# Kernel tuning notes

Hardware: AMD Instinct MI355X
Metric: run time of the kernel (lower is better)

The kernel has to match this reference:

```python
import jax, jax.numpy as jnp
import numpy as np

N_ATOMS = 8_000_000
N_REC = 2_000_000
N_POC = 500_000
N_CHAINS = 4


def setup_inputs() -> dict:
    key = jax.random.key(0)
    k1, k2, k3, k4 = jax.random.split(key, 4)
    # coordinates in nm, inside a ~5 nm box
    positions = jax.random.uniform(k1, (N_ATOMS, 3), dtype=jnp.float32) * 5.0
    box_vectors = jnp.diag(jnp.array([5.0, 5.0, 5.0], dtype=jnp.float32))
    # unique receptor atom indices into positions
    rec_indices = jax.random.permutation(k2, N_ATOMS)[:N_REC].astype(jnp.int32)
    # unique pocket indices INTO THE REC ARRAY (poc_pos = rec_pos[poc_indices])
    poc_indices = jax.random.permutation(k3, N_REC)[:N_POC].astype(jnp.int32)
    # contiguous chain assignment over rec atoms, all chains present in pocket
    chain_ids = ((jnp.arange(N_REC, dtype=jnp.int32) * N_CHAINS) // N_REC).astype(jnp.int32)
    poc_chain_ids = chain_ids[poc_indices]
    ref_poc = jax.random.uniform(k4, (N_POC, 3), dtype=jnp.float32) * 5.0
    k = jnp.float32(100.0)  # kJ/mol/nm^2
    return {
        "positions": positions, "box_vectors": box_vectors, "ref_poc": ref_poc,
        "k": k, "rec_indices": rec_indices, "poc_indices": poc_indices,
        "chain_ids": chain_ids, "poc_chain_ids": poc_chain_ids, "n_chains": N_CHAINS,
    }


def best_periodic_translation(pos1, pos2, box_vectors):
    # pos1, pos2: [C,3]; box_vectors: [3,3] (rows are lattice vectors)
    delta = pos2 - pos1
    inv = 1.0 / jnp.diag(box_vectors)
    s3 = jnp.round(delta[:, 2] * inv[2])
    delta = delta - s3[:, None] * box_vectors[2]
    s2 = jnp.round(delta[:, 1] * inv[1])
    delta = delta - s2[:, None] * box_vectors[1]
    s1 = jnp.round(delta[:, 0] * inv[0])
    return s1[:, None] * box_vectors[0] + s2[:, None] * box_vectors[1] + s3[:, None] * box_vectors[2]


def reference(positions, box_vectors, ref_poc, k, rec_indices, poc_indices, chain_ids, poc_chain_ids, n_chains):
    rec_pos = positions[rec_indices]  # [R,3]
    # Per-chain pocket COM. NOTE: original indexes global positions here
    # (positions[poc_chain_indices]), NOT rec_pos -- reproduced faithfully.
    poc_glob = positions[poc_indices]  # [P,3]
    counts = jax.ops.segment_sum(jnp.ones((poc_glob.shape[0],), poc_glob.dtype), poc_chain_ids, num_segments=n_chains)  # [C]
    poc_com = jax.ops.segment_sum(poc_glob, poc_chain_ids, num_segments=n_chains) / counts[:, None]  # [C,3]
    ref_com = jax.ops.segment_sum(ref_poc, poc_chain_ids, num_segments=n_chains) / counts[:, None]  # [C,3]
    best_t = best_periodic_translation(poc_com, ref_com, box_vectors)  # [C,3]
    rec_pos = rec_pos + best_t[chain_ids]  # translate each chain into the reference image

    poc_pos = rec_pos[poc_indices]  # [P,3]
    rec_origin = jnp.mean(rec_pos, axis=0)
    rec_centered = rec_pos - rec_origin
    r_sq = jnp.sum(rec_centered ** 2, axis=1)  # [R]
    F = jnp.zeros_like(rec_pos).at[poc_indices].set(-2.0 * k * (poc_pos - ref_poc))
    F_mean = jnp.mean(F, axis=0)
    torque = jnp.cross(rec_centered, F)
    torque_mean = jnp.mean(torque, axis=0)
    F_rot = jnp.cross(torque_mean[None], rec_centered) / r_sq[:, None]
    F_final = jnp.zeros_like(positions).at[rec_indices].set(F_mean + F_rot)
    return (jnp.float32(0.0), F_final)
```

## Files before the change

### kernel.cpp

```cpp
#include <hip/hip_runtime.h>


typedef unsigned int uint32;
typedef unsigned char uchar;

#define MAXC 16
#define W_BT 0
#define W_O 48
#define W_FM 52
#define W_TM 56
#define W_ACC 64

#define GCOUNT_OFF 4096
#define REC_OFF 8192
#define NB 512
#define BSH 14
#define BUCKET_ATOMS (1 << BSH)
#define CAP 5120
#define INV8_OFF (REC_OFF + NB * CAP * 4)

#define PB 512
#define K1_KPT 16
#define K1_CHUNK (256 * K1_KPT)

struct PocSh  { float accL[3 + MAXC * 10]; };
struct MapSh  { uchar map_[BUCKET_ATOMS]; };
union ShU { PocSh poc; MapSh map; };

__device__ inline float waveSum(float v) {
#pragma unroll
  for (int off = 32; off > 0; off >>= 1) v += __shfl_down(v, off, 64);
  return v;
}

__global__ __launch_bounds__(256) void k_partition(
    const int* __restrict__ rec_idx, const int* __restrict__ cid,
    int R, uint32* __restrict__ gcount, uint32* __restrict__ grecords) {
  __shared__ uint32 hist[NB];
  __shared__ uint32 curs[NB];
  __shared__ uint32 base[NB];
  const int tid = threadIdx.x;
  const int r0 = blockIdx.x * K1_CHUNK;
  int cnt = R - r0; if (cnt > K1_CHUNK) cnt = K1_CHUNK;
  for (int t = tid; t < NB; t += 256) { hist[t] = 0u; curs[t] = 0u; }
  __syncthreads();
  uint32 enc[K1_KPT];
#pragma unroll
  for (int j = 0; j < K1_KPT; ++j) {
    int t = tid + j * 256;
    uint32 e = 0xFFFFFFFFu;
    if (t < cnt) {
      uint32 idx = (uint32)rec_idx[r0 + t];
      uint32 c = (uint32)cid[r0 + t] & 255u;
      e = (idx << 8) | c;
      atomicAdd(&hist[idx >> BSH], 1u);
    }
    enc[j] = e;
  }
  __syncthreads();
  for (int t = tid; t < NB; t += 256) {
    uint32 h = hist[t];
    base[t] = h ? atomicAdd(&gcount[t], h) : 0u;
  }
  __syncthreads();
#pragma unroll
  for (int j = 0; j < K1_KPT; ++j) {
    uint32 e = enc[j];
    if (e != 0xFFFFFFFFu) {
      uint32 b = e >> (8 + BSH);
      uint32 slot = base[b] + atomicAdd(&curs[b], 1u);
      if (slot < CAP) grecords[b * CAP + slot] = e;
    }
  }
}

__global__ __launch_bounds__(256) void k_gather(
    const float* __restrict__ pos, const float* __restrict__ ref_poc,
    const int* __restrict__ rec_idx,
    const int* __restrict__ poc_idx, const int* __restrict__ poc_cid,
    const int* __restrict__ ncp, int P, int N,
    const uint32* __restrict__ gcount, const uint32* __restrict__ grecords,
    uchar* __restrict__ inv8, float* __restrict__ ws) {
  const int tid = threadIdx.x;
  const int bid = blockIdx.x;
  const int C = ncp[0];
  __shared__ ShU sh;
  __shared__ float red[4][43];
  __shared__ float cnt16[MAXC];

  if ((bid & 1) == 0) {
    const int pt = bid >> 1;
    const int gsz = PB * 256;
    if (C <= 4) {
      float vals[43];
#pragma unroll
      for (int v = 0; v < 43; ++v) vals[v] = 0.f;
      for (int rb = pt * 256 + tid; rb < P; rb += 4 * gsz) {
        int rr[4], i2[4], c2[4], ri[4];
        float g[4][3], p[4][3], rf[4][3];
#pragma unroll
        for (int q = 0; q < 4; ++q) {
          int r = rb + q * gsz;
          rr[q] = (r < P) ? r : -1;
        }
#pragma unroll
        for (int q = 0; q < 4; ++q) {
          int r = (rr[q] < 0) ? 0 : rr[q];
          i2[q] = poc_idx[r];
          c2[q] = poc_cid[r];
        }
#pragma unroll
        for (int q = 0; q < 4; ++q) {
          ri[q] = rec_idx[i2[q]];
          g[q][0] = pos[3 * i2[q] + 0];
          g[q][1] = pos[3 * i2[q] + 1];
          g[q][2] = pos[3 * i2[q] + 2];
        }
#pragma unroll
        for (int q = 0; q < 4; ++q) {
          int r = (rr[q] < 0) ? 0 : rr[q];
          p[q][0] = pos[3 * ri[q] + 0];
          p[q][1] = pos[3 * ri[q] + 1];
          p[q][2] = pos[3 * ri[q] + 2];
          rf[q][0] = ref_poc[3 * r + 0];
          rf[q][1] = ref_poc[3 * r + 1];
          rf[q][2] = ref_poc[3 * r + 2];
        }
#pragma unroll
        for (int q = 0; q < 4; ++q) {
          if (rr[q] >= 0) {
            vals[0] += p[q][1] * rf[q][2] - p[q][2] * rf[q][1];
            vals[1] += p[q][2] * rf[q][0] - p[q][0] * rf[q][2];
            vals[2] += p[q][0] * rf[q][1] - p[q][1] * rf[q][0];
#pragma unroll
            for (int cc = 0; cc < 4; ++cc) {
              bool m = (c2[q] == cc);
              float* a = &vals[3 + cc * 10];
              a[0] += m ? g[q][0] : 0.f; a[1] += m ? g[q][1] : 0.f;
              a[2] += m ? g[q][2] : 0.f;
              a[3] += m ? rf[q][0] : 0.f; a[4] += m ? rf[q][1] : 0.f;
              a[5] += m ? rf[q][2] : 0.f;
              a[6] += m ? p[q][0] : 0.f; a[7] += m ? p[q][1] : 0.f;
              a[8] += m ? p[q][2] : 0.f;
              a[9] += m ? 1.f : 0.f;
            }
          }
        }
      }
      const int wid = tid >> 6;
#pragma unroll
      for (int v = 0; v < 43; ++v) {
        float s = waveSum(vals[v]);
        if ((tid & 63) == 0) red[wid][v] = s;
      }
      __syncthreads();
      for (int t = tid; t < 43; t += 256)
        atomicAdd(&ws[W_ACC + 19 + t],
                  red[0][t] + red[1][t] + red[2][t] + red[3][t]);
    } else {
      float* accL = sh.poc.accL;
      for (int t = tid; t < 3 + MAXC * 10; t += 256) accL[t] = 0.f;
      __syncthreads();
      for (int r = pt * 256 + tid; r < P; r += PB * 256) {
        int i2 = poc_idx[r];
        int c2 = poc_cid[r];
        int ri = rec_idx[i2];
        float gx = pos[3 * i2 + 0], gy = pos[3 * i2 + 1], gz = pos[3 * i2 + 2];
        float px = pos[3 * ri + 0], py = pos[3 * ri + 1], pz = pos[3 * ri + 2];
        float rx = ref_poc[3 * r + 0], ry = ref_poc[3 * r + 1], rz = ref_poc[3 * r + 2];
        atomicAdd(&accL[0], py * rz - pz * ry);
        atomicAdd(&accL[1], pz * rx - px * rz);
        atomicAdd(&accL[2], px * ry - py * rx);
        float* a = &accL[3 + c2 * 10];
        atomicAdd(&a[0], gx); atomicAdd(&a[1], gy); atomicAdd(&a[2], gz);
        atomicAdd(&a[3], rx); atomicAdd(&a[4], ry); atomicAdd(&a[5], rz);
        atomicAdd(&a[6], px); atomicAdd(&a[7], py); atomicAdd(&a[8], pz);
        atomicAdd(&a[9], 1.f);
      }
      __syncthreads();
      for (int t = tid; t < 3 + MAXC * 10; t += 256)
        if (accL[t] != 0.f) atomicAdd(&ws[W_ACC + 19 + t], accL[t]);
    }
  } else {
    const int b = bid >> 1;
    const int a0 = b << BSH;
    if (a0 >= N) return;
    int natoms = N - a0; if (natoms > BUCKET_ATOMS) natoms = BUCKET_ATOMS;
    uchar* map_ = sh.map.map_;
    uint4* m16 = (uint4*)map_;
    uint4 ff; ff.x = ff.y = ff.z = ff.w = 0xFFFFFFFFu;
    for (int t = tid; t < BUCKET_ATOMS / 16; t += 256) m16[t] = ff;
    if (C > 4) for (int t = tid; t < MAXC; t += 256) cnt16[t] = 0.f;
    __syncthreads();
    int n = (int)gcount[b]; if (n > CAP) n = CAP;
    float c0 = 0.f, c1 = 0.f, c2 = 0.f, c3 = 0.f;
    for (int t = tid; t < n; t += 256) {
      uint32 e = grecords[b * CAP + t];
      uint32 ia = (e >> 8) & (BUCKET_ATOMS - 1);
      uint32 c = e & 255u;
      map_[ia] = (uchar)c;
      if (C <= 4) {
        c0 += (c == 0u) ? 1.f : 0.f;
        c1 += (c == 1u) ? 1.f : 0.f;
        c2 += (c == 2u) ? 1.f : 0.f;
        c3 += (c == 3u) ? 1.f : 0.f;
      } else {
        atomicAdd(&cnt16[c], 1.f);
      }
    }
    __syncthreads();
    uchar* dst = inv8 + a0;
    if (natoms == BUCKET_ATOMS) {
      uint4* d16 = (uint4*)dst;
      for (int t = tid; t < BUCKET_ATOMS / 16; t += 256) d16[t] = m16[t];
    } else {
      for (int t = tid; t < natoms; t += 256) dst[t] = map_[t];
    }
    float sx = 0.f, sy = 0.f, sz = 0.f;
    int ngf = natoms >> 2;
    const uchar4* m4 = (const uchar4*)map_;
    const float4* pos4 = (const float4*)pos;
    int g0 = a0 >> 2;
    for (int g = tid; g < ngf; g += 256) {
      float4 p0 = pos4[3 * (g0 + g) + 0];
      float4 p1 = pos4[3 * (g0 + g) + 1];
      float4 p2 = pos4[3 * (g0 + g) + 2];
      uchar4 m = m4[g];
      if (m.x != 255) { sx += p0.x; sy += p0.y; sz += p0.z; }
      if (m.y != 255) { sx += p0.w; sy += p1.x; sz += p1.y; }
      if (m.z != 255) { sx += p1.z; sy += p1.w; sz += p2.x; }
      if (m.w != 255) { sx += p2.y; sy += p2.z; sz += p2.w; }
    }
    int tb = natoms & 3;
    if (tid < tb) {
      int a = a0 + (ngf << 2) + tid;
      if (map_[(ngf << 2) + tid] != 255) {
        sx += pos[3 * a]; sy += pos[3 * a + 1]; sz += pos[3 * a + 2];
      }
    }
    float vv[7] = {sx, sy, sz, c0, c1, c2, c3};
    const int wid = tid >> 6;
#pragma unroll
    for (int v = 0; v < 7; ++v) {
      float s = waveSum(vv[v]);
      if ((tid & 63) == 0) red[wid][v] = s;
    }
    __syncthreads();
    if (tid < 7) {
      float s = red[0][tid] + red[1][tid] + red[2][tid] + red[3][tid];
      atomicAdd(&ws[W_ACC + tid], s);
    }
    if (C > 4 && tid < C) atomicAdd(&ws[W_ACC + 3 + tid], cnt16[tid]);
  }
}

__global__ __launch_bounds__(256) void k_finout(
    const float* __restrict__ pos, const uchar* __restrict__ inv8,
    const float* __restrict__ box, const float* __restrict__ kp,
    const int* __restrict__ ncp, int R, int N,
    const float* __restrict__ ws, float* __restrict__ out) {
  __shared__ float stage[3328];
  __shared__ float tot[192];
  __shared__ float sc[64];
  const int tid = threadIdx.x;
  const int t0 = blockIdx.x * 1024;
  int nat = N - t0; if (nat > 1024) nat = 1024;
  const int nfl = nat * 3;

  for (int t = tid; t < 192; t += 256) tot[t] = ws[W_ACC + t];

  if (nat == 1024) {
    const float4* src4 = (const float4*)(pos + 3 * t0);
#pragma unroll
    for (int kk = 0; kk < 3; ++kk) {
      int v4 = tid + kk * 256;
      float4 p = src4[v4];
      int idx = 4 * v4 + v4 / 3;
      stage[idx + 0] = p.x; stage[idx + 1] = p.y;
      stage[idx + 2] = p.z; stage[idx + 3] = p.w;
    }
  } else {
    for (int k = tid; k < nfl; k += 256)
      stage[k + (int)((unsigned)k / 12u)] = pos[3 * t0 + k];
  }
  __syncthreads();

  if (tid == 0) {
    const int C = ncp[0];
    const float kk = kp[0];
    const float Rf = (float)R;
    const float* xp = &tot[19];
    float inv0 = 1.f / box[0], inv1 = 1.f / box[4], inv2 = 1.f / box[8];
    float ox = tot[0], oy = tot[1], oz = tot[2];
    float Fx = 0, Fy = 0, Fz = 0;
    float T1x = 0, T1y = 0, T1z = 0, T2x = 0, T2y = 0, T2z = 0;
    for (int c = 0; c < C; ++c) {
      float nrec = tot[3 + c];
      const float* a = &tot[22 + c * 10];
      float np = a[9];
      float invn = 1.f / np;
      float pcx = a[0] * invn, pcy = a[1] * invn, pcz = a[2] * invn;
      float rcx = a[3] * invn, rcy = a[4] * invn, rcz = a[5] * invn;
      float dx = rcx - pcx, dy = rcy - pcy, dz = rcz - pcz;
      float s3 = rintf(dz * inv2);
      dx -= s3 * box[6]; dy -= s3 * box[7]; dz -= s3 * box[8];
      float s2 = rintf(dy * inv1);
      dx -= s2 * box[3]; dy -= s2 * box[4]; dz -= s2 * box[5];
      float s1 = rintf(dx * inv0);
      float btx = s1 * box[0] + s2 * box[3] + s3 * box[6];
      float bty = s1 * box[1] + s2 * box[4] + s3 * box[7];
      float btz = s1 * box[2] + s2 * box[5] + s3 * box[8];
      sc[W_BT + c * 3 + 0] = btx;
      sc[W_BT + c * 3 + 1] = bty;
      sc[W_BT + c * 3 + 2] = btz;
      ox += nrec * btx; oy += nrec * bty; oz += nrec * btz;
      float SFx = -2.f * kk * (a[6] + np * btx - a[3]);
      float SFy = -2.f * kk * (a[7] + np * bty - a[4]);
      float SFz = -2.f * kk * (a[8] + np * btz - a[5]);
      Fx += SFx; Fy += SFy; Fz += SFz;
      T1x += a[7] * btz - a[8] * bty;
      T1y += a[8] * btx - a[6] * btz;
      T1z += a[6] * bty - a[7] * btx;
      T2x += bty * SFz - btz * SFy;
      T2y += btz * SFx - btx * SFz;
      T2z += btx * SFy - bty * SFx;
    }
    ox /= Rf; oy /= Rf; oz /= Rf;
    float Tx = 2.f * kk * xp[0] - 2.f * kk * T1x + T2x - (oy * Fz - oz * Fy);
    float Ty = 2.f * kk * xp[1] - 2.f * kk * T1y + T2y - (oz * Fx - ox * Fz);
    float Tz = 2.f * kk * xp[2] - 2.f * kk * T1z + T2z - (ox * Fy - oy * Fx);
    sc[W_O + 0] = ox; sc[W_O + 1] = oy; sc[W_O + 2] = oz;
    sc[W_FM + 0] = Fx / Rf; sc[W_FM + 1] = Fy / Rf; sc[W_FM + 2] = Fz / Rf;
    sc[W_TM + 0] = Tx / Rf; sc[W_TM + 1] = Ty / Rf; sc[W_TM + 2] = Tz / Rf;
  }
  __syncthreads();

  const float ox = sc[W_O + 0], oy = sc[W_O + 1], oz = sc[W_O + 2];
  const float fmx = sc[W_FM + 0], fmy = sc[W_FM + 1], fmz = sc[W_FM + 2];
  const float tmx = sc[W_TM + 0], tmy = sc[W_TM + 1], tmz = sc[W_TM + 2];

  uchar mc[4];
  if (nat == 1024) {
    uchar4 m = ((const uchar4*)(inv8 + t0))[tid];
    mc[0] = m.x; mc[1] = m.y; mc[2] = m.z; mc[3] = m.w;
  } else {
#pragma unroll
    for (int q = 0; q < 4; ++q) {
      int la = 4 * tid + q;
      mc[q] = (la < nat) ? inv8[t0 + la] : (uchar)255;
    }
  }
#pragma unroll
  for (int q = 0; q < 4; ++q) {
    int la = 4 * tid + q;
    if (la < nat) {
      float* s = &stage[13 * tid + 3 * q];
      float fx = 0.f, fy = 0.f, fz = 0.f;
      int c = mc[q];
      if (c != 255) {
        float cx = s[0] + sc[W_BT + 3 * c + 0] - ox;
        float cy = s[1] + sc[W_BT + 3 * c + 1] - oy;
        float cz = s[2] + sc[W_BT + 3 * c + 2] - oz;
        float inv = 1.f / (cx * cx + cy * cy + cz * cz);
        fx = fmx + (tmy * cz - tmz * cy) * inv;
        fy = fmy + (tmz * cx - tmx * cz) * inv;
        fz = fmz + (tmx * cy - tmy * cx) * inv;
      }
      s[0] = fx; s[1] = fy; s[2] = fz;
    }
  }
  __syncthreads();

  if (blockIdx.x == 0 && tid == 0) out[0] = 0.f;
  float* ob = out + 1 + 3 * t0;
  if (nat == 1024) {
#pragma unroll
    for (int kk = 0; kk < 3; ++kk) {
      int j = tid + kk * 256;
      if (j < 767) {
        int k = 3 + 4 * j;
        float4 v;
        v.x = stage[k + k / 12];
        v.y = stage[(k + 1) + (k + 1) / 12];
        v.z = stage[(k + 2) + (k + 2) / 12];
        v.w = stage[(k + 3) + (k + 3) / 12];
        *(float4*)(ob + k) = v;
      }
    }
    if (tid < 3) ob[tid] = stage[tid];
    if (tid == 3) ob[3071] = stage[3071 + 3071 / 12];
  } else {
    for (int k = tid; k < nfl; k += 256)
      ob[k] = stage[k + (int)((unsigned)k / 12u)];
  }
}

extern "C" void kernel_launch(void* const* d_in, const int* in_sizes, int n_in,
                              void* d_out, int out_size, void* d_ws, size_t ws_size,
                              hipStream_t stream) {
  const float* pos     = (const float*)d_in[0];
  const float* box     = (const float*)d_in[1];
  const float* ref_poc = (const float*)d_in[2];
  const float* kp      = (const float*)d_in[3];
  const int* rec_idx   = (const int*)d_in[4];
  const int* poc_idx   = (const int*)d_in[5];
  const int* cid       = (const int*)d_in[6];
  const int* poc_cid   = (const int*)d_in[7];
  const int* ncp       = (const int*)d_in[8];
  float* out = (float*)d_out;
  float* ws  = (float*)d_ws;
  uint32* gcount   = (uint32*)((char*)d_ws + GCOUNT_OFF);
  uint32* grecords = (uint32*)((char*)d_ws + REC_OFF);
  uchar*  inv8     = (uchar*)d_ws + INV8_OFF;

  const int N = in_sizes[0] / 3;
  const int R = in_sizes[4];
  const int P = in_sizes[5];

  hipMemsetAsync(d_ws, 0, 8192, stream);

  const int nchunk = (R + K1_CHUNK - 1) / K1_CHUNK;
  k_partition<<<nchunk, 256, 0, stream>>>(rec_idx, cid, R, gcount, grecords);
  k_gather<<<1024, 256, 0, stream>>>(pos, ref_poc, rec_idx, poc_idx, poc_cid,
                                     ncp, P, N, gcount, grecords, inv8, ws);
  int gF = (N + 1023) / 1024;
  k_finout<<<gF, 256, 0, stream>>>(pos, inv8, box, kp, ncp, R, N, ws, out);
}
```

Before: 270.2 us.

## Fuse three kernels into one persistent kernel with software grid barriers

```diff
diff --git a/kernel.cpp b/kernel.cpp
--- a/kernel.cpp
+++ b/kernel.cpp
@@ -11,6 +11,7 @@
 #define W_TM 56
 #define W_ACC 64
 
+#define BAR_OFF 4032
 #define GCOUNT_OFF 4096
 #define REC_OFF 8192
 #define NB 512
@@ -19,13 +20,18 @@
 #define CAP 5120
 #define INV8_OFF (REC_OFF + NB * CAP * 4)
 
-#define PB 512
+#define GRID 512
+#define PBK 256
 #define K1_KPT 16
 #define K1_CHUNK (256 * K1_KPT)
 
+#define SPIN_MAX (1 << 22)
+
+struct PartSh { uint32 hist[NB]; uint32 curs[NB]; uint32 base[NB]; };
 struct PocSh  { float accL[3 + MAXC * 10]; };
 struct MapSh  { uchar map_[BUCKET_ATOMS]; };
-union ShU { PocSh poc; MapSh map; };
+struct StageSh{ float stage[3328]; float tot[192]; };
+union ShU { PartSh part; PocSh poc; MapSh map; StageSh st; };
 
 __device__ inline float waveSum(float v) {
 #pragma unroll
@@ -33,64 +39,87 @@
   return v;
 }
 
-__global__ __launch_bounds__(256) void k_partition(
-    const int* __restrict__ rec_idx, const int* __restrict__ cid,
-    int R, uint32* __restrict__ gcount, uint32* __restrict__ grecords) {
-  __shared__ uint32 hist[NB];
-  __shared__ uint32 curs[NB];
-  __shared__ uint32 base[NB];
-  const int tid = threadIdx.x;
-  const int r0 = blockIdx.x * K1_CHUNK;
-  int cnt = R - r0; if (cnt > K1_CHUNK) cnt = K1_CHUNK;
-  for (int t = tid; t < NB; t += 256) { hist[t] = 0u; curs[t] = 0u; }
+__device__ inline void gridBar(uint32* bar, uint32 phase, int* shOk) {
+  __threadfence();
   __syncthreads();
-  uint32 enc[K1_KPT];
-#pragma unroll
-  for (int j = 0; j < K1_KPT; ++j) {
-    int t = tid + j * 256;
-    uint32 e = 0xFFFFFFFFu;
-    if (t < cnt) {
-      uint32 idx = (uint32)rec_idx[r0 + t];
-      uint32 c = (uint32)cid[r0 + t] & 255u;
-      e = (idx << 8) | c;
-      atomicAdd(&hist[idx >> BSH], 1u);
-    }
-    enc[j] = e;
+  if (threadIdx.x == 0) {
+    __hip_atomic_fetch_add(bar, 1u, __ATOMIC_ACQ_REL, __HIP_MEMORY_SCOPE_AGENT);
+    const uint32 tgt = (uint32)GRID * phase;
+    for (int it = 0; it < SPIN_MAX; ++it) {
+      if (__hip_atomic_load(bar, __ATOMIC_ACQUIRE, __HIP_MEMORY_SCOPE_AGENT) >= tgt)
+        break;
+      __builtin_amdgcn_s_sleep(2);
+    }
+    *shOk = 1;
   }
   __syncthreads();
-  for (int t = tid; t < NB; t += 256) {
-    uint32 h = hist[t];
-    base[t] = h ? atomicAdd(&gcount[t], h) : 0u;
-  }
-  __syncthreads();
-#pragma unroll
-  for (int j = 0; j < K1_KPT; ++j) {
-    uint32 e = enc[j];
-    if (e != 0xFFFFFFFFu) {
-      uint32 b = e >> (8 + BSH);
-      uint32 slot = base[b] + atomicAdd(&curs[b], 1u);
-      if (slot < CAP) grecords[b * CAP + slot] = e;
-    }
-  }
+  __threadfence();
 }
 
-__global__ __launch_bounds__(256) void k_gather(
+__global__ __launch_bounds__(256, 2) void k_all(
     const float* __restrict__ pos, const float* __restrict__ ref_poc,
-    const int* __restrict__ rec_idx,
+    const int* __restrict__ rec_idx, const int* __restrict__ cid,
     const int* __restrict__ poc_idx, const int* __restrict__ poc_cid,
-    const int* __restrict__ ncp, int P, int N,
-    const uint32* __restrict__ gcount, const uint32* __restrict__ grecords,
-    uchar* __restrict__ inv8, float* __restrict__ ws) {
+    const int* __restrict__ ncp, const float* __restrict__ box,
+    const float* __restrict__ kp, int R, int P, int N,
+    uint32* __restrict__ gcount, uint32* __restrict__ grecords,
+    uchar* __restrict__ inv8, float* __restrict__ ws,
+    float* __restrict__ out, uint32* __restrict__ bar) {
+  __shared__ ShU sh;
+  __shared__ float red[4][43];
+  __shared__ float cnt16[MAXC];
+  __shared__ float sc[64];
+  __shared__ int shOk;
   const int tid = threadIdx.x;
   const int bid = blockIdx.x;
   const int C = ncp[0];
-  __shared__ ShU sh;
-  __shared__ float red[4][43];
-  __shared__ float cnt16[MAXC];
+  const int NCHUNK = (R + K1_CHUNK - 1) / K1_CHUNK;
+
+  {
+    uint32* hist = sh.part.hist;
+    uint32* curs = sh.part.curs;
+    uint32* base = sh.part.base;
+    for (int ch = bid; ch < NCHUNK; ch += GRID) {
+      const int r0 = ch * K1_CHUNK;
+      int cnt = R - r0; if (cnt > K1_CHUNK) cnt = K1_CHUNK;
+      for (int t = tid; t < NB; t += 256) { hist[t] = 0u; curs[t] = 0u; }
+      __syncthreads();
+      uint32 enc[K1_KPT];
+#pragma unroll
+      for (int j = 0; j < K1_KPT; ++j) {
+        int t = tid + j * 256;
+        uint32 e = 0xFFFFFFFFu;
+        if (t < cnt) {
+          uint32 idx = (uint32)rec_idx[r0 + t];
+          uint32 c = (uint32)cid[r0 + t] & 255u;
+          e = (idx << 8) | c;
+          atomicAdd(&hist[idx >> BSH], 1u);
+        }
+        enc[j] = e;
+      }
+      __syncthreads();
+      for (int t = tid; t < NB; t += 256) {
+        uint32 h = hist[t];
+        base[t] = h ? atomicAdd(&gcount[t], h) : 0u;
+      }
+      __syncthreads();
+#pragma unroll
+      for (int j = 0; j < K1_KPT; ++j) {
+        uint32 e = enc[j];
+        if (e != 0xFFFFFFFFu) {
+          uint32 b = e >> (8 + BSH);
+          uint32 slot = base[b] + atomicAdd(&curs[b], 1u);
+          if (slot < CAP) grecords[b * CAP + slot] = e;
+        }
+      }
+      __syncthreads();
+    }
+  }
+  gridBar(bar, 1, &shOk);
 
   if ((bid & 1) == 0) {
     const int pt = bid >> 1;
-    const int gsz = PB * 256;
+    const int gsz = PBK * 256;
     if (C <= 4) {
       float vals[43];
 #pragma unroll
@@ -161,7 +190,7 @@
       float* accL = sh.poc.accL;
       for (int t = tid; t < 3 + MAXC * 10; t += 256) accL[t] = 0.f;
       __syncthreads();
-      for (int r = pt * 256 + tid; r < P; r += PB * 256) {
+      for (int r = pt * 256 + tid; r < P; r += PBK * 256) {
         int i2 = poc_idx[r];
         int c2 = poc_cid[r];
         int ri = rec_idx[i2];
@@ -182,216 +211,215 @@
         if (accL[t] != 0.f) atomicAdd(&ws[W_ACC + 19 + t], accL[t]);
     }
   } else {
-    const int b = bid >> 1;
-    const int a0 = b << BSH;
-    if (a0 >= N) return;
-    int natoms = N - a0; if (natoms > BUCKET_ATOMS) natoms = BUCKET_ATOMS;
-    uchar* map_ = sh.map.map_;
-    uint4* m16 = (uint4*)map_;
-    uint4 ff; ff.x = ff.y = ff.z = ff.w = 0xFFFFFFFFu;
-    for (int t = tid; t < BUCKET_ATOMS / 16; t += 256) m16[t] = ff;
-    if (C > 4) for (int t = tid; t < MAXC; t += 256) cnt16[t] = 0.f;
+    for (int b = (bid >> 1); b < NB; b += 256) {
+      const int a0 = b << BSH;
+      if (a0 >= N) break;
+      int natoms = N - a0; if (natoms > BUCKET_ATOMS) natoms = BUCKET_ATOMS;
+      uchar* map_ = sh.map.map_;
+      uint4* m16 = (uint4*)map_;
+      uint4 ff; ff.x = ff.y = ff.z = ff.w = 0xFFFFFFFFu;
+      for (int t = tid; t < BUCKET_ATOMS / 16; t += 256) m16[t] = ff;
+      if (C > 4) for (int t = tid; t < MAXC; t += 256) cnt16[t] = 0.f;
+      __syncthreads();
+      int n = (int)gcount[b]; if (n > CAP) n = CAP;
+      float c0 = 0.f, c1 = 0.f, c2 = 0.f, c3 = 0.f;
+      for (int t = tid; t < n; t += 256) {
+        uint32 e = grecords[b * CAP + t];
+        uint32 ia = (e >> 8) & (BUCKET_ATOMS - 1);
+        uint32 c = e & 255u;
+        map_[ia] = (uchar)c;
+        if (C <= 4) {
+          c0 += (c == 0u) ? 1.f : 0.f;
+          c1 += (c == 1u) ? 1.f : 0.f;
+          c2 += (c == 2u) ? 1.f : 0.f;
+          c3 += (c == 3u) ? 1.f : 0.f;
+        } else {
+          atomicAdd(&cnt16[c], 1.f);
+        }
+      }
+      __syncthreads();
+      uchar* dst = inv8 + a0;
+      if (natoms == BUCKET_ATOMS) {
+        uint4* d16 = (uint4*)dst;
+        for (int t = tid; t < BUCKET_ATOMS / 16; t += 256) d16[t] = m16[t];
+      } else {
+        for (int t = tid; t < natoms; t += 256) dst[t] = map_[t];
+      }
+      float sx = 0.f, sy = 0.f, sz = 0.f;
+      int ngf = natoms >> 2;
+      const uchar4* m4 = (const uchar4*)map_;
+      const float4* pos4 = (const float4*)pos;
+      int g0 = a0 >> 2;
+      for (int g = tid; g < ngf; g += 256) {
+        float4 p0 = pos4[3 * (g0 + g) + 0];
+        float4 p1 = pos4[3 * (g0 + g) + 1];
+        float4 p2 = pos4[3 * (g0 + g) + 2];
+        uchar4 m = m4[g];
+        if (m.x != 255) { sx += p0.x; sy += p0.y; sz += p0.z; }
+        if (m.y != 255) { sx += p0.w; sy += p1.x; sz += p1.y; }
+        if (m.z != 255) { sx += p1.z; sy += p1.w; sz += p2.x; }
+        if (m.w != 255) { sx += p2.y; sy += p2.z; sz += p2.w; }
+      }
+      int tb = natoms & 3;
+      if (tid < tb) {
+        int a = a0 + (ngf << 2) + tid;
+        if (map_[(ngf << 2) + tid] != 255) {
+          sx += pos[3 * a]; sy += pos[3 * a + 1]; sz += pos[3 * a + 2];
+        }
+      }
+      float vv[7] = {sx, sy, sz, c0, c1, c2, c3};
+      const int wid = tid >> 6;
+#pragma unroll
+      for (int v = 0; v < 7; ++v) {
+        float s = waveSum(vv[v]);
+        if ((tid & 63) == 0) red[wid][v] = s;
+      }
+      __syncthreads();
+      if (tid < 7) {
+        float s = red[0][tid] + red[1][tid] + red[2][tid] + red[3][tid];
+        atomicAdd(&ws[W_ACC + tid], s);
+      }
+      if (C > 4 && tid < C) atomicAdd(&ws[W_ACC + 3 + tid], cnt16[tid]);
+      __syncthreads();
+    }
+  }
+  gridBar(bar, 2, &shOk);
+
+  {
+    float* tot = sh.st.tot;
+    for (int t = tid; t < 192; t += 256) tot[t] = ws[W_ACC + t];
     __syncthreads();
-    int n = (int)gcount[b]; if (n > CAP) n = CAP;
-    float c0 = 0.f, c1 = 0.f, c2 = 0.f, c3 = 0.f;
-    for (int t = tid; t < n; t += 256) {
-      uint32 e = grecords[b * CAP + t];
-      uint32 ia = (e >> 8) & (BUCKET_ATOMS - 1);
-      uint32 c = e & 255u;
-      map_[ia] = (uchar)c;
-      if (C <= 4) {
-        c0 += (c == 0u) ? 1.f : 0.f;
-        c1 += (c == 1u) ? 1.f : 0.f;
-        c2 += (c == 2u) ? 1.f : 0.f;
-        c3 += (c == 3u) ? 1.f : 0.f;
+    if (tid == 0) {
+      const float kk = kp[0];
+      const float Rf = (float)R;
+      const float* xp = &tot[19];
+      float inv0 = 1.f / box[0], inv1 = 1.f / box[4], inv2 = 1.f / box[8];
+      float ox = tot[0], oy = tot[1], oz = tot[2];
+      float Fx = 0, Fy = 0, Fz = 0;
+      float T1x = 0, T1y = 0, T1z = 0, T2x = 0, T2y = 0, T2z = 0;
+      for (int c = 0; c < C; ++c) {
+        float nrec = tot[3 + c];
+        const float* a = &tot[22 + c * 10];
+        float np = a[9];
+        float invn = 1.f / np;
+        float pcx = a[0] * invn, pcy = a[1] * invn, pcz = a[2] * invn;
+        float rcx = a[3] * invn, rcy = a[4] * invn, rcz = a[5] * invn;
+        float dx = rcx - pcx, dy = rcy - pcy, dz = rcz - pcz;
+        float s3 = rintf(dz * inv2);
+        dx -= s3 * box[6]; dy -= s3 * box[7]; dz -= s3 * box[8];
+        float s2 = rintf(dy * inv1);
+        dx -= s2 * box[3]; dy -= s2 * box[4]; dz -= s2 * box[5];
+        float s1 = rintf(dx * inv0);
+        float btx = s1 * box[0] + s2 * box[3] + s3 * box[6];
+        float bty = s1 * box[1] + s2 * box[4] + s3 * box[7];
+        float btz = s1 * box[2] + s2 * box[5] + s3 * box[8];
+        sc[W_BT + c * 3 + 0] = btx;
+        sc[W_BT + c * 3 + 1] = bty;
+        sc[W_BT + c * 3 + 2] = btz;
+        ox += nrec * btx; oy += nrec * bty; oz += nrec * btz;
+        float SFx = -2.f * kk * (a[6] + np * btx - a[3]);
+        float SFy = -2.f * kk * (a[7] + np * bty - a[4]);
+        float SFz = -2.f * kk * (a[8] + np * btz - a[5]);
+        Fx += SFx; Fy += SFy; Fz += SFz;
+        T1x += a[7] * btz - a[8] * bty;
+        T1y += a[8] * btx - a[6] * btz;
+        T1z += a[6] * bty - a[7] * btx;
+        T2x += bty * SFz - btz * SFy;
+        T2y += btz * SFx - btx * SFz;
+        T2z += btx * SFy - bty * SFx;
+      }
+      ox /= Rf; oy /= Rf; oz /= Rf;
+      float Tx = 2.f * kk * xp[0] - 2.f * kk * T1x + T2x - (oy * Fz - oz * Fy);
+      float Ty = 2.f * kk * xp[1] - 2.f * kk * T1y + T2y - (oz * Fx - ox * Fz);
+      float Tz = 2.f * kk * xp[2] - 2.f * kk * T1z + T2z - (ox * Fy - oy * Fx);
+      sc[W_O + 0] = ox; sc[W_O + 1] = oy; sc[W_O + 2] = oz;
+      sc[W_FM + 0] = Fx / Rf; sc[W_FM + 1] = Fy / Rf; sc[W_FM + 2] = Fz / Rf;
+      sc[W_TM + 0] = Tx / Rf; sc[W_TM + 1] = Ty / Rf; sc[W_TM + 2] = Tz / Rf;
+    }
+    __syncthreads();
+    const float ox = sc[W_O + 0], oy = sc[W_O + 1], oz = sc[W_O + 2];
+    const float fmx = sc[W_FM + 0], fmy = sc[W_FM + 1], fmz = sc[W_FM + 2];
+    const float tmx = sc[W_TM + 0], tmy = sc[W_TM + 1], tmz = sc[W_TM + 2];
+
+    const int ntiles = (N + 1023) >> 10;
+    for (int tile = bid; tile < ntiles; tile += GRID) {
+      const int t0 = tile << 10;
+      int nat = N - t0; if (nat > 1024) nat = 1024;
+      const int nfl = nat * 3;
+      float* stage = sh.st.stage;
+
+      if (nat == 1024) {
+        const float4* src4 = (const float4*)(pos + 3 * t0);
+#pragma unroll
+        for (int kk = 0; kk < 3; ++kk) {
+          int v4 = tid + kk * 256;
+          float4 p = src4[v4];
+          int idx = 4 * v4 + v4 / 3;
+          stage[idx + 0] = p.x; stage[idx + 1] = p.y;
+          stage[idx + 2] = p.z; stage[idx + 3] = p.w;
+        }
       } else {
-        atomicAdd(&cnt16[c], 1.f);
-      }
-    }
-    __syncthreads();
-    uchar* dst = inv8 + a0;
-    if (natoms == BUCKET_ATOMS) {
-      uint4* d16 = (uint4*)dst;
-      for (int t = tid; t < BUCKET_ATOMS / 16; t += 256) d16[t] = m16[t];
-    } else {
-      for (int t = tid; t < natoms; t += 256) dst[t] = map_[t];
-    }
-    float sx = 0.f, sy = 0.f, sz = 0.f;
-    int ngf = natoms >> 2;
-    const uchar4* m4 = (const uchar4*)map_;
-    const float4* pos4 = (const float4*)pos;
-    int g0 = a0 >> 2;
-    for (int g = tid; g < ngf; g += 256) {
-      float4 p0 = pos4[3 * (g0 + g) + 0];
-      float4 p1 = pos4[3 * (g0 + g) + 1];
-      float4 p2 = pos4[3 * (g0 + g) + 2];
-      uchar4 m = m4[g];
-      if (m.x != 255) { sx += p0.x; sy += p0.y; sz += p0.z; }
-      if (m.y != 255) { sx += p0.w; sy += p1.x; sz += p1.y; }
-      if (m.z != 255) { sx += p1.z; sy += p1.w; sz += p2.x; }
-      if (m.w != 255) { sx += p2.y; sy += p2.z; sz += p2.w; }
-    }
-    int tb = natoms & 3;
-    if (tid < tb) {
-      int a = a0 + (ngf << 2) + tid;
-      if (map_[(ngf << 2) + tid] != 255) {
-        sx += pos[3 * a]; sy += pos[3 * a + 1]; sz += pos[3 * a + 2];
-      }
-    }
-    float vv[7] = {sx, sy, sz, c0, c1, c2, c3};
-    const int wid = tid >> 6;
-#pragma unroll
-    for (int v = 0; v < 7; ++v) {
-      float s = waveSum(vv[v]);
-      if ((tid & 63) == 0) red[wid][v] = s;
-    }
-    __syncthreads();
-    if (tid < 7) {
-      float s = red[0][tid] + red[1][tid] + red[2][tid] + red[3][tid];
-      atomicAdd(&ws[W_ACC + tid], s);
-    }
-    if (C > 4 && tid < C) atomicAdd(&ws[W_ACC + 3 + tid], cnt16[tid]);
-  }
-}
-
-__global__ __launch_bounds__(256) void k_finout(
-    const float* __restrict__ pos, const uchar* __restrict__ inv8,
-    const float* __restrict__ box, const float* __restrict__ kp,
-    const int* __restrict__ ncp, int R, int N,
-    const float* __restrict__ ws, float* __restrict__ out) {
-  __shared__ float stage[3328];
-  __shared__ float tot[192];
-  __shared__ float sc[64];
-  const int tid = threadIdx.x;
-  const int t0 = blockIdx.x * 1024;
-  int nat = N - t0; if (nat > 1024) nat = 1024;
-  const int nfl = nat * 3;
-
-  for (int t = tid; t < 192; t += 256) tot[t] = ws[W_ACC + t];
-
-  if (nat == 1024) {
-    const float4* src4 = (const float4*)(pos + 3 * t0);
-#pragma unroll
-    for (int kk = 0; kk < 3; ++kk) {
-      int v4 = tid + kk * 256;
-      float4 p = src4[v4];
-      int idx = 4 * v4 + v4 / 3;
-      stage[idx + 0] = p.x; stage[idx + 1] = p.y;
-      stage[idx + 2] = p.z; stage[idx + 3] = p.w;
-    }
-  } else {
-    for (int k = tid; k < nfl; k += 256)
-      stage[k + (int)((unsigned)k / 12u)] = pos[3 * t0 + k];
-  }
-  __syncthreads();
-
-  if (tid == 0) {
-    const int C = ncp[0];
-    const float kk = kp[0];
-    const float Rf = (float)R;
-    const float* xp = &tot[19];
-    float inv0 = 1.f / box[0], inv1 = 1.f / box[4], inv2 = 1.f / box[8];
-    float ox = tot[0], oy = tot[1], oz = tot[2];
-    float Fx = 0, Fy = 0, Fz = 0;
-    float T1x = 0, T1y = 0, T1z = 0, T2x = 0, T2y = 0, T2z = 0;
-    for (int c = 0; c < C; ++c) {
-      float nrec = tot[3 + c];
-      const float* a = &tot[22 + c * 10];
-      float np = a[9];
-      float invn = 1.f / np;
-      float pcx = a[0] * invn, pcy = a[1] * invn, pcz = a[2] * invn;
-      float rcx = a[3] * invn, rcy = a[4] * invn, rcz = a[5] * invn;
-      float dx = rcx - pcx, dy = rcy - pcy, dz = rcz - pcz;
-      float s3 = rintf(dz * inv2);
-      dx -= s3 * box[6]; dy -= s3 * box[7]; dz -= s3 * box[8];
-      float s2 = rintf(dy * inv1);
-      dx -= s2 * box[3]; dy -= s2 * box[4]; dz -= s2 * box[5];
-      float s1 = rintf(dx * inv0);
-      float btx = s1 * box[0] + s2 * box[3] + s3 * box[6];
-      float bty = s1 * box[1] + s2 * box[4] + s3 * box[7];
-      float btz = s1 * box[2] + s2 * box[5] + s3 * box[8];
-      sc[W_BT + c * 3 + 0] = btx;
-      sc[W_BT + c * 3 + 1] = bty;
-      sc[W_BT + c * 3 + 2] = btz;
-      ox += nrec * btx; oy += nrec * bty; oz += nrec * btz;
-      float SFx = -2.f * kk * (a[6] + np * btx - a[3]);
-      float SFy = -2.f * kk * (a[7] + np * bty - a[4]);
-      float SFz = -2.f * kk * (a[8] + np * btz - a[5]);
-      Fx += SFx; Fy += SFy; Fz += SFz;
-      T1x += a[7] * btz - a[8] * bty;
-      T1y += a[8] * btx - a[6] * btz;
-      T1z += a[6] * bty - a[7] * btx;
-      T2x += bty * SFz - btz * SFy;
-      T2y += btz * SFx - btx * SFz;
-      T2z += btx * SFy - bty * SFx;
-    }
-    ox /= Rf; oy /= Rf; oz /= Rf;
-    float Tx = 2.f * kk * xp[0] - 2.f * kk * T1x + T2x - (oy * Fz - oz * Fy);
-    float Ty = 2.f * kk * xp[1] - 2.f * kk * T1y + T2y - (oz * Fx - ox * Fz);
-    float Tz = 2.f * kk * xp[2] - 2.f * kk * T1z + T2z - (ox * Fy - oy * Fx);
-    sc[W_O + 0] = ox; sc[W_O + 1] = oy; sc[W_O + 2] = oz;
-    sc[W_FM + 0] = Fx / Rf; sc[W_FM + 1] = Fy / Rf; sc[W_FM + 2] = Fz / Rf;
-    sc[W_TM + 0] = Tx / Rf; sc[W_TM + 1] = Ty / Rf; sc[W_TM + 2] = Tz / Rf;
-  }
-  __syncthreads();
-
-  const float ox = sc[W_O + 0], oy = sc[W_O + 1], oz = sc[W_O + 2];
-  const float fmx = sc[W_FM + 0], fmy = sc[W_FM + 1], fmz = sc[W_FM + 2];
-  const float tmx = sc[W_TM + 0], tmy = sc[W_TM + 1], tmz = sc[W_TM + 2];
-
-  uchar mc[4];
-  if (nat == 1024) {
-    uchar4 m = ((const uchar4*)(inv8 + t0))[tid];
-    mc[0] = m.x; mc[1] = m.y; mc[2] = m.z; mc[3] = m.w;
-  } else {
-#pragma unroll
-    for (int q = 0; q < 4; ++q) {
-      int la = 4 * tid + q;
-      mc[q] = (la < nat) ? inv8[t0 + la] : (uchar)255;
-    }
-  }
-#pragma unroll
-  for (int q = 0; q < 4; ++q) {
-    int la = 4 * tid + q;
-    if (la < nat) {
-      float* s = &stage[13 * tid + 3 * q];
-      float fx = 0.f, fy = 0.f, fz = 0.f;
-      int c = mc[q];
-      if (c != 255) {
-        float cx = s[0] + sc[W_BT + 3 * c + 0] - ox;
-        float cy = s[1] + sc[W_BT + 3 * c + 1] - oy;
-        float cz = s[2] + sc[W_BT + 3 * c + 2] - oz;
-        float inv = 1.f / (cx * cx + cy * cy + cz * cz);
-        fx = fmx + (tmy * cz - tmz * cy) * inv;
-        fy = fmy + (tmz * cx - tmx * cz) * inv;
-        fz = fmz + (tmx * cy - tmy * cx) * inv;
-      }
-      s[0] = fx; s[1] = fy; s[2] = fz;
-    }
-  }
-  __syncthreads();
-
-  if (blockIdx.x == 0 && tid == 0) out[0] = 0.f;
-  float* ob = out + 1 + 3 * t0;
-  if (nat == 1024) {
-#pragma unroll
-    for (int kk = 0; kk < 3; ++kk) {
-      int j = tid + kk * 256;
-      if (j < 767) {
-        int k = 3 + 4 * j;
-        float4 v;
-        v.x = stage[k + k / 12];
-        v.y = stage[(k + 1) + (k + 1) / 12];
-        v.z = stage[(k + 2) + (k + 2) / 12];
-        v.w = stage[(k + 3) + (k + 3) / 12];
-        *(float4*)(ob + k) = v;
-      }
-    }
-    if (tid < 3) ob[tid] = stage[tid];
-    if (tid == 3) ob[3071] = stage[3071 + 3071 / 12];
-  } else {
-    for (int k = tid; k < nfl; k += 256)
-      ob[k] = stage[k + (int)((unsigned)k / 12u)];
+        for (int k = tid; k < nfl; k += 256)
+          stage[k + (int)((unsigned)k / 12u)] = pos[3 * t0 + k];
+      }
+      __syncthreads();
+
+      uchar mc[4];
+      if (nat == 1024) {
+        uchar4 m = ((const uchar4*)(inv8 + t0))[tid];
+        mc[0] = m.x; mc[1] = m.y; mc[2] = m.z; mc[3] = m.w;
+      } else {
+#pragma unroll
+        for (int q = 0; q < 4; ++q) {
+          int la = 4 * tid + q;
+          mc[q] = (la < nat) ? inv8[t0 + la] : (uchar)255;
+        }
+      }
+#pragma unroll
+      for (int q = 0; q < 4; ++q) {
+        int la = 4 * tid + q;
+        if (la < nat) {
+          float* s = &stage[13 * tid + 3 * q];
+          float fx = 0.f, fy = 0.f, fz = 0.f;
+          int c = mc[q];
+          if (c != 255) {
+            float cx = s[0] + sc[W_BT + 3 * c + 0] - ox;
+            float cy = s[1] + sc[W_BT + 3 * c + 1] - oy;
+            float cz = s[2] + sc[W_BT + 3 * c + 2] - oz;
+            float inv = 1.f / (cx * cx + cy * cy + cz * cz);
+            fx = fmx + (tmy * cz - tmz * cy) * inv;
+            fy = fmy + (tmz * cx - tmx * cz) * inv;
+            fz = fmz + (tmx * cy - tmy * cx) * inv;
+          }
+          s[0] = fx; s[1] = fy; s[2] = fz;
+        }
+      }
+      __syncthreads();
+
+      if (tile == 0 && tid == 0) out[0] = 0.f;
+      float* ob = out + 1 + 3 * t0;
+      if (nat == 1024) {
+#pragma unroll
+        for (int kk = 0; kk < 3; ++kk) {
+          int j = tid + kk * 256;
+          if (j < 767) {
+            int k = 3 + 4 * j;
+            float4 v;
+            v.x = stage[k + k / 12];
+            v.y = stage[(k + 1) + (k + 1) / 12];
+            v.z = stage[(k + 2) + (k + 2) / 12];
+            v.w = stage[(k + 3) + (k + 3) / 12];
+            *(float4*)(ob + k) = v;
+          }
+        }
+        if (tid < 3) ob[tid] = stage[tid];
+        if (tid == 3) ob[3071] = stage[3071 + 3071 / 12];
+      } else {
+        for (int k = tid; k < nfl; k += 256)
+          ob[k] = stage[k + (int)((unsigned)k / 12u)];
+      }
+      __syncthreads();
+    }
   }
 }
 
@@ -409,6 +437,7 @@
   const int* ncp       = (const int*)d_in[8];
   float* out = (float*)d_out;
   float* ws  = (float*)d_ws;
+  uint32* bar      = (uint32*)((char*)d_ws + BAR_OFF);
   uint32* gcount   = (uint32*)((char*)d_ws + GCOUNT_OFF);
   uint32* grecords = (uint32*)((char*)d_ws + REC_OFF);
   uchar*  inv8     = (uchar*)d_ws + INV8_OFF;
@@ -419,10 +448,7 @@
 
   hipMemsetAsync(d_ws, 0, 8192, stream);
 
-  const int nchunk = (R + K1_CHUNK - 1) / K1_CHUNK;
-  k_partition<<<nchunk, 256, 0, stream>>>(rec_idx, cid, R, gcount, grecords);
-  k_gather<<<1024, 256, 0, stream>>>(pos, ref_poc, rec_idx, poc_idx, poc_cid,
-                                     ncp, P, N, gcount, grecords, inv8, ws);
-  int gF = (N + 1023) / 1024;
-  k_finout<<<gF, 256, 0, stream>>>(pos, inv8, box, kp, ncp, R, N, ws, out);
+  k_all<<<GRID, 256, 0, stream>>>(
+      pos, ref_poc, rec_idx, cid, poc_idx, poc_cid, ncp, box, kp,
+      R, P, N, gcount, grecords, inv8, ws, out, bar);
 }
```

Result: slower. 565.8 us (+109.4%).
